# Optimization experiments

Measured on AMD Instinct MI355X. Metric: run time of the kernel, lower is better.

Reference implementation:

```python
import jax, jax.numpy as jnp
import numpy as np

N_SEND = 100000   # sender nodes
N_RECV = 100000   # receiver nodes
E = 600000        # edges
D = 128           # node feature channels (128x0e)
A = 8             # attr channels (8x0e)
S = 64            # edge scalar dim = fc_neurons[0]
H = 128           # fc hidden = fc_neurons[1]; tp.weight_numel = 128
NUM_NEIGHBORS = 32.0
SILU_NORM = 1.679177  # e3nn normalize2mom constant for silu: (E[silu(N(0,1))^2])^-0.5


def fctp(x, y, W):
    """e3nn FullyConnectedTensorProduct for all-scalar (0e) irreps:
    single 'uvw' path, path weight 1/sqrt(mul_u*mul_v)."""
    return jnp.einsum('nu,nv,uvw->nw', x, y, W) / np.sqrt(x.shape[1] * y.shape[1]).astype(np.float32)


def setup_inputs() -> dict:
    key = jax.random.key(0)
    ks = jax.random.split(key, 14)
    return {
        'sender_input': jax.random.normal(ks[0], (N_SEND, D), jnp.float32),
        'sender_attr': jax.random.normal(ks[1], (N_SEND, A), jnp.float32),
        'receiver_input': jax.random.normal(ks[2], (N_RECV, D), jnp.float32),
        'receiver_attr': jax.random.normal(ks[3], (N_RECV, A), jnp.float32),
        'edge_src': jax.random.randint(ks[4], (E,), 0, N_SEND, jnp.int32),
        'edge_dst': jax.random.randint(ks[5], (E,), 0, N_RECV, jnp.int32),
        'edge_attr': jax.random.normal(ks[6], (E, 1), jnp.float32),
        'edge_scalars': jax.random.normal(ks[7], (E, S), jnp.float32),
        # e3nn TP weights are initialized N(0,1)
        'W_sc': jax.random.normal(ks[8], (D, A, D), jnp.float32),
        'W_lin1': jax.random.normal(ks[9], (D, A, D), jnp.float32),
        'W_fc1': jax.random.normal(ks[10], (S, H), jnp.float32),
        'W_fc2': jax.random.normal(ks[11], (H, D), jnp.float32),
        'W_lin2': jax.random.normal(ks[12], (D, A, D), jnp.float32),
        'W_lin3': jax.random.normal(ks[13], (D, A, 1), jnp.float32),
    }


def reference(sender_input, sender_attr, receiver_input, receiver_attr,
              edge_src, edge_dst, edge_attr, edge_scalars,
              W_sc, W_lin1, W_fc1, W_fc2, W_lin2, W_lin3):
    # FullyConnectedNet([S, H, weight_numel], silu): act(x@W/sqrt(fan_in)), last layer linear
    h = SILU_NORM * jax.nn.silu(edge_scalars @ W_fc1 / np.sqrt(S).astype(np.float32))
    weight = h @ W_fc2 / np.sqrt(H).astype(np.float32)                     # [E, D] per-edge TP weights

    receiver_self_connection = fctp(receiver_input, receiver_attr, W_sc)   # [Nr, D]
    sender_features = fctp(sender_input, sender_attr, W_lin1)              # [Ns, D]

    # gather -> per-edge weighted ('uvu') tensor product with 1x0e edge_attr -> scatter-add
    edge_features = weight * sender_features[edge_src] * edge_attr         # [E, D]
    receiver_features = jax.ops.segment_sum(edge_features, edge_dst,
                                            num_segments=receiver_input.shape[0])
    receiver_features = receiver_features / np.sqrt(NUM_NEIGHBORS).astype(np.float32)

    receiver_conv_out = fctp(receiver_features, receiver_attr, W_lin2)     # [Nr, D]
    receiver_angle = 0.1 * fctp(receiver_features, receiver_attr, W_lin3)  # [Nr, 1]
    # sc.output_mask is all-ones for this irreps config, so sin gating applies to all channels
    return jnp.cos(receiver_angle) * receiver_self_connection + jnp.sin(receiver_angle) * receiver_conv_out
```

## Files before the change

### kernel.cpp

```cpp
#include <hip/hip_runtime.h>
#include <hip/hip_bf16.h>
#include <math.h>

#define NS 100000
#define NR 100000
#define NE 600000
#define SILU_NORM 1.679177f

typedef __attribute__((ext_vector_type(8))) short short8;
typedef __attribute__((ext_vector_type(4))) float f32x4;

static __device__ __forceinline__ short f2bf(float f) {
    return __builtin_bit_cast(short, __float2bfloat16(f));
}

#define GLDS16(g, l)                                                         \
    __builtin_amdgcn_global_load_lds(                                        \
        (const __attribute__((address_space(1))) unsigned int*)(const void*)(g), \
        (__attribute__((address_space(3))) unsigned int*)(void*)(l), 16, 0, 0)

__global__ void swz_kernel(const float* __restrict__ W,
                           __hip_bfloat16* __restrict__ out, int total)
{
    int idx = blockIdx.x * 256 + threadIdx.x;
    if (idx >= total) return;
    int s = idx >> 12, r = idx & 4095;
    int f = r >> 9;  r &= 511;
    int quad = r >> 7; r &= 127;
    int wl = r >> 3;
    int j = r & 7;
    int k = s * 32 + quad * 8 + j;
    int w = f * 16 + wl;
    out[idx] = __float2bfloat16(W[(size_t)k * 128 + w]);
}

__global__ __launch_bounds__(256) void hist_kernel(const int* __restrict__ edst,
                                                   int* __restrict__ cnt)
{
    int i = blockIdx.x * 256 + threadIdx.x;
    if (i < NE) atomicAdd(&cnt[edst[i]], 1);
}

#define SCAN_BLK 1024

__global__ __launch_bounds__(256) void scan1_kernel(const int* __restrict__ cnt,
                                                    int* __restrict__ bsum, int n)
{
    __shared__ int ts[256];
    int b = blockIdx.x, t = threadIdx.x;
    int base = b * SCAN_BLK + t * 4;
    int s = 0;
    #pragma unroll
    for (int k = 0; k < 4; ++k) { int i = base + k; if (i < n) s += cnt[i]; }
    ts[t] = s; __syncthreads();
    #pragma unroll
    for (int off = 128; off; off >>= 1) {
        if (t < off) ts[t] += ts[t + off];
        __syncthreads();
    }
    if (t == 0) bsum[b] = ts[0];
}

__global__ __launch_bounds__(128) void scan2_kernel(const int* __restrict__ bsum,
                                                    int* __restrict__ bofs, int nb)
{
    __shared__ int sh[128];
    int t = threadIdx.x;
    sh[t] = (t < nb) ? bsum[t] : 0;
    __syncthreads();
    for (int off = 1; off < 128; off <<= 1) {
        int v = (t >= off) ? sh[t - off] : 0;
        __syncthreads();
        sh[t] += v;
        __syncthreads();
    }
    if (t < nb) bofs[t] = (t == 0) ? 0 : sh[t - 1];
}

__global__ __launch_bounds__(256) void scan3_kernel(const int* __restrict__ cnt,
                                                    const int* __restrict__ bofs,
                                                    int* __restrict__ ofs, int n)
{
    __shared__ int ts[256];
    int b = blockIdx.x, t = threadIdx.x;
    int base = b * SCAN_BLK + t * 4;
    int v[4]; int s = 0;
    #pragma unroll
    for (int k = 0; k < 4; ++k) {
        int i = base + k;
        v[k] = (i < n) ? cnt[i] : 0;
        s += v[k];
    }
    ts[t] = s; __syncthreads();
    for (int off = 1; off < 256; off <<= 1) {
        int u = (t >= off) ? ts[t - off] : 0;
        __syncthreads();
        ts[t] += u;
        __syncthreads();
    }
    int run = bofs[b] + ts[t] - s;
    #pragma unroll
    for (int k = 0; k < 4; ++k) {
        int i = base + k;
        if (i < n) ofs[i] = run;
        run += v[k];
    }
}

__global__ __launch_bounds__(256) void scatter_kernel(const int* __restrict__ edst,
                                                      int* __restrict__ ofs,
                                                      int* __restrict__ perm)
{
    int i = blockIdx.x * 256 + threadIdx.x;
    if (i < NE) {
        int pos = atomicAdd(&ofs[edst[i]], 1);
        perm[pos] = i;
    }
}

__global__ __launch_bounds__(256) void fctp_mfma_kernel(
    const float* __restrict__ x, const float* __restrict__ y,
    const __hip_bfloat16* __restrict__ Wswz, float* __restrict__ out,
    float scale, int N)
{
    __shared__ __hip_bfloat16 Wb[2][8192];
    __shared__ float xs[2][128 * 8];

    const int tid = threadIdx.x;
    const int lane = tid & 63;
    const int wv = tid >> 6;
    const int quad = lane >> 4;
    const int wl = lane & 15;
    const int n0 = blockIdx.x * 128;

    float ya[2][8];
    #pragma unroll
    for (int mt = 0; mt < 2; ++mt) {
        int node = n0 + wv * 32 + mt * 16 + wl;
        if (node >= N) node = N - 1;
        const float4* yp = (const float4*)(y + (size_t)node * 8);
        float4 a = yp[0], b = yp[1];
        ya[mt][0] = a.x; ya[mt][1] = a.y; ya[mt][2] = a.z; ya[mt][3] = a.w;
        ya[mt][4] = b.x; ya[mt][5] = b.y; ya[mt][6] = b.z; ya[mt][7] = b.w;
    }

    f32x4 acc[2][8];
    #pragma unroll
    for (int mt = 0; mt < 2; ++mt)
        #pragma unroll
        for (int f = 0; f < 8; ++f)
            acc[mt][f] = (f32x4){0.f, 0.f, 0.f, 0.f};

    auto stage = [&](int b, int cc) {
        const char* src = (const char*)(Wswz + (size_t)cc * 8192);
        #pragma unroll
        for (int i = 0; i < 4; ++i) {
            int off = (i * 256 + tid) * 16;
            GLDS16(src + off, (char*)Wb[b] + off);
        }
        int nl = tid >> 1, c4 = (tid & 1) * 4;
        int node = n0 + nl;
        if (node >= N) node = N - 1;
        GLDS16(x + (size_t)node * 128 + cc * 8 + c4, (char*)xs[b] + tid * 16);
    };

    stage(0, 0);
    __syncthreads();

    for (int cc = 0; cc < 16; ++cc) {
        int cur = cc & 1;
        if (cc < 15) stage(cur ^ 1, cc + 1);

        #pragma unroll
        for (int ks = 0; ks < 2; ++ks) {
            short8 bfr[8];
            #pragma unroll
            for (int f = 0; f < 8; ++f)
                bfr[f] = *(const short8*)((const short*)Wb[cur] +
                                          (size_t)ks * 4096 + (f * 64 + lane) * 8);
            #pragma unroll
            for (int mt = 0; mt < 2; ++mt) {
                float xv = xs[cur][(wv * 32 + mt * 16 + wl) * 8 + ks * 4 + quad];
                short8 af;
                #pragma unroll
                for (int v = 0; v < 8; ++v) af[v] = f2bf(xv * ya[mt][v]);
                #pragma unroll
                for (int f = 0; f < 8; ++f)
                    acc[mt][f] = __builtin_amdgcn_mfma_f32_16x16x32_bf16(
                        af, bfr[f], acc[mt][f], 0, 0, 0);
            }
        }
        __syncthreads();
    }

    #pragma unroll
    for (int mt = 0; mt < 2; ++mt) {
        #pragma unroll
        for (int r = 0; r < 4; ++r) {
            int node = n0 + wv * 32 + mt * 16 + quad * 4 + r;
            if (node < N) {
                #pragma unroll
                for (int f = 0; f < 8; ++f)
                    out[(size_t)node * 128 + f * 16 + wl] = acc[mt][f][r] * scale;
            }
        }
    }
}

__global__ __launch_bounds__(256, 4) void edge_mfma_kernel(
    const int* __restrict__ esrc, const int* __restrict__ edst,
    const float* __restrict__ eattr, const float* __restrict__ escal,
    const int* __restrict__ perm,
    const __hip_bfloat16* __restrict__ W1swz,
    const __hip_bfloat16* __restrict__ W2swz,
    const float* __restrict__ sf, float* __restrict__ rfeat)
{
    __shared__ __hip_bfloat16 hA[16384];

    const int tid = threadIdx.x;
    const int lane = tid & 63;
    const int wv = tid >> 6;
    const int quad = lane >> 4;
    const int wl = lane & 15;
    const int e0 = blockIdx.x * 128;

    int epm[2];
    #pragma unroll
    for (int mt = 0; mt < 2; ++mt) {
        int j = e0 + (wv * 2 + mt) * 16 + wl;
        if (j >= NE) j = NE - 1;
        epm[mt] = perm[j];
    }

    short8 af1[2][2];
    #pragma unroll
    for (int ks = 0; ks < 2; ++ks)
        #pragma unroll
        for (int mt = 0; mt < 2; ++mt) {
            const float4* p = (const float4*)(escal + (size_t)epm[mt] * 64 +
                                              ks * 32 + quad * 8);
            float4 a = p[0], b = p[1];
            short8 v;
            v[0] = f2bf(a.x); v[1] = f2bf(a.y); v[2] = f2bf(a.z); v[3] = f2bf(a.w);
            v[4] = f2bf(b.x); v[5] = f2bf(b.y); v[6] = f2bf(b.z); v[7] = f2bf(b.w);
            af1[ks][mt] = v;
        }

    f32x4 acc1[2][8];
    #pragma unroll
    for (int mt = 0; mt < 2; ++mt)
        #pragma unroll
        for (int f = 0; f < 8; ++f) acc1[mt][f] = (f32x4){0.f, 0.f, 0.f, 0.f};

    #pragma unroll
    for (int ks = 0; ks < 2; ++ks)
        #pragma unroll
        for (int f = 0; f < 8; ++f) {
            short8 bfr = *(const short8*)((const short*)W1swz +
                                          (size_t)ks * 4096 + (f * 64 + lane) * 8);
            acc1[0][f] = __builtin_amdgcn_mfma_f32_16x16x32_bf16(
                af1[0][0], bfr, acc1[0][f], 0, 0, 0);
            acc1[1][f] = __builtin_amdgcn_mfma_f32_16x16x32_bf16(
                af1[0][1], bfr, acc1[1][f], 0, 0, 0);
        }

    #pragma unroll
    for (int mt = 0; mt < 2; ++mt)
        #pragma unroll
        for (int f = 0; f < 8; ++f) acc1[mt][f] = (f32x4){0.f, 0.f, 0.f, 0.f};
    #pragma unroll
    for (int ks = 0; ks < 2; ++ks)
        #pragma unroll
        for (int f = 0; f < 8; ++f) {
            short8 bfr = *(const short8*)((const short*)W1swz +
                                          (size_t)ks * 4096 + (f * 64 + lane) * 8);
            acc1[0][f] = __builtin_amdgcn_mfma_f32_16x16x32_bf16(
                af1[ks][0], bfr, acc1[0][f], 0, 0, 0);
            acc1[1][f] = __builtin_amdgcn_mfma_f32_16x16x32_bf16(
                af1[ks][1], bfr, acc1[1][f], 0, 0, 0);
        }

    #pragma unroll
    for (int mt = 0; mt < 2; ++mt) {
        int MT = wv * 2 + mt;
        #pragma unroll
        for (int f = 0; f < 8; ++f) {
            int s2 = f >> 1;
            int q2 = ((f & 1) * 2 + (wl >> 3)) & 3;
            int j2 = wl & 7;
            #pragma unroll
            for (int r = 0; r < 4; ++r) {
                float t = acc1[mt][f][r] * 0.125f;
                float h = SILU_NORM * t / (1.f + __expf(-t));
                int lpos = q2 * 16 + quad * 4 + r;
                ((short*)hA)[((size_t)(s2 * 8 + MT) * 64 + lpos) * 8 + j2] = f2bf(h);
            }
        }
    }
    __syncthreads();

    f32x4 acc2[2][8];
    #pragma unroll
    for (int mt = 0; mt < 2; ++mt)
        #pragma unroll
        for (int f = 0; f < 8; ++f) acc2[mt][f] = (f32x4){0.f, 0.f, 0.f, 0.f};

    #pragma unroll
    for (int ks = 0; ks < 4; ++ks) {
        short8 afA = *(const short8*)((const short*)hA +
                                      ((size_t)(ks * 8 + wv * 2 + 0) * 64 + lane) * 8);
        short8 afB = *(const short8*)((const short*)hA +
                                      ((size_t)(ks * 8 + wv * 2 + 1) * 64 + lane) * 8);
        #pragma unroll
        for (int f = 0; f < 8; ++f) {
            short8 bfr = *(const short8*)((const short*)W2swz +
                                          (size_t)ks * 4096 + (f * 64 + lane) * 8);
            acc2[0][f] = __builtin_amdgcn_mfma_f32_16x16x32_bf16(
                afA, bfr, acc2[0][f], 0, 0, 0);
            acc2[1][f] = __builtin_amdgcn_mfma_f32_16x16x32_bf16(
                afB, bfr, acc2[1][f], 0, 0, 0);
        }
    }

    const float s128 = 0.08838834764831845f;
    #pragma unroll
    for (int mt = 0; mt < 2; ++mt) {
        int jbase = e0 + (wv * 2 + mt) * 16 + quad * 4;
        if (jbase < NE) {
            int4 pj = *(const int4*)(perm + jbase);
            int dsts[4], srcs[4];
            float eas[4];
            #pragma unroll
            for (int r = 0; r < 4; ++r) {
                int e = (r == 0) ? pj.x : (r == 1) ? pj.y : (r == 2) ? pj.z : pj.w;
                dsts[r] = edst[e];
                srcs[r] = esrc[e];
                eas[r]  = eattr[e] * s128;
            }
            float run[8];
            int curdst = dsts[0];
            #pragma unroll
            for (int f = 0; f < 8; ++f)
                run[f] = acc2[mt][f][0] * eas[0] *
                         sf[(size_t)srcs[0] * 128 + f * 16 + wl];
            #pragma unroll
            for (int r = 1; r < 4; ++r) {
                float val[8];
                #pragma unroll
                for (int f = 0; f < 8; ++f)
                    val[f] = acc2[mt][f][r] * eas[r] *
                             sf[(size_t)srcs[r] * 128 + f * 16 + wl];
                if (dsts[r] == curdst) {
                    #pragma unroll
                    for (int f = 0; f < 8; ++f) run[f] += val[f];
                } else {
                    #pragma unroll
                    for (int f = 0; f < 8; ++f)
                        atomicAdd(&rfeat[(size_t)curdst * 128 + f * 16 + wl], run[f]);
                    curdst = dsts[r];
                    #pragma unroll
                    for (int f = 0; f < 8; ++f) run[f] = val[f];
                }
            }
            #pragma unroll
            for (int f = 0; f < 8; ++f)
                atomicAdd(&rfeat[(size_t)curdst * 128 + f * 16 + wl], run[f]);
        }
    }
}

__global__ __launch_bounds__(256) void conv_fuse_kernel(
    const float* __restrict__ x, const float* __restrict__ y,
    const __hip_bfloat16* __restrict__ Wswz, const float* __restrict__ W3,
    const float* __restrict__ rsc, float* __restrict__ out, int N)
{
    __shared__ __hip_bfloat16 Wb[2][8192];
    __shared__ float xs[2][128 * 8];

    const int tid = threadIdx.x;
    const int lane = tid & 63;
    const int wv = tid >> 6;
    const int quad = lane >> 4;
    const int wl = lane & 15;
    const int n0 = blockIdx.x * 128;

    float ya[2][8];
    #pragma unroll
    for (int mt = 0; mt < 2; ++mt) {
        int node = n0 + wv * 32 + mt * 16 + wl;
        if (node >= N) node = N - 1;
        const float4* yp = (const float4*)(y + (size_t)node * 8);
        float4 a = yp[0], b = yp[1];
        ya[mt][0] = a.x; ya[mt][1] = a.y; ya[mt][2] = a.z; ya[mt][3] = a.w;
        ya[mt][4] = b.x; ya[mt][5] = b.y; ya[mt][6] = b.z; ya[mt][7] = b.w;
    }

    f32x4 acc[2][8];
    #pragma unroll
    for (int mt = 0; mt < 2; ++mt)
        #pragma unroll
        for (int f = 0; f < 8; ++f)
            acc[mt][f] = (f32x4){0.f, 0.f, 0.f, 0.f};
    float aacc[2] = {0.f, 0.f};

    auto stage = [&](int b, int cc) {
        const char* src = (const char*)(Wswz + (size_t)cc * 8192);
        #pragma unroll
        for (int i = 0; i < 4; ++i) {
            int off = (i * 256 + tid) * 16;
            GLDS16(src + off, (char*)Wb[b] + off);
        }
        int nl = tid >> 1, c4 = (tid & 1) * 4;
        int node = n0 + nl;
        if (node >= N) node = N - 1;
        GLDS16(x + (size_t)node * 128 + cc * 8 + c4, (char*)xs[b] + tid * 16);
    };

    stage(0, 0);
    __syncthreads();

    for (int cc = 0; cc < 16; ++cc) {
        int cur = cc & 1;
        if (cc < 15) stage(cur ^ 1, cc + 1);

        #pragma unroll
        for (int ks = 0; ks < 2; ++ks) {
            short8 bfr[8];
            #pragma unroll
            for (int f = 0; f < 8; ++f)
                bfr[f] = *(const short8*)((const short*)Wb[cur] +
                                          (size_t)ks * 4096 + (f * 64 + lane) * 8);
            const float4* wp = (const float4*)(W3 + ((cc * 8 + ks * 4 + quad) * 8));
            float4 w3a = wp[0], w3b = wp[1];
            float w3v[8] = {w3a.x, w3a.y, w3a.z, w3a.w, w3b.x, w3b.y, w3b.z, w3b.w};
            #pragma unroll
            for (int mt = 0; mt < 2; ++mt) {
                float xv = xs[cur][(wv * 32 + mt * 16 + wl) * 8 + ks * 4 + quad];
                short8 af;
                #pragma unroll
                for (int v = 0; v < 8; ++v) {
                    float pr = xv * ya[mt][v];
                    af[v] = f2bf(pr);
                    aacc[mt] += pr * w3v[v];
                }
                #pragma unroll
                for (int f = 0; f < 8; ++f)
                    acc[mt][f] = __builtin_amdgcn_mfma_f32_16x16x32_bf16(
                        af, bfr[f], acc[mt][f], 0, 0, 0);
            }
        }
        __syncthreads();
    }

    float ared[2];
    #pragma unroll
    for (int mt = 0; mt < 2; ++mt) {
        float a = aacc[mt];
        a += __shfl_xor(a, 16);
        a += __shfl_xor(a, 32);
        ared[mt] = a * 5.524271728019903e-4f;
    }

    const float cs = 5.524271728019903e-3f;
    #pragma unroll
    for (int mt = 0; mt < 2; ++mt) {
        #pragma unroll
        for (int r = 0; r < 4; ++r) {
            int node = n0 + wv * 32 + mt * 16 + quad * 4 + r;
            float a = __shfl(ared[mt], quad * 4 + r);
            if (node < N) {
                float ca = __cosf(a), sa = __sinf(a);
                #pragma unroll
                for (int f = 0; f < 8; ++f) {
                    size_t o = (size_t)node * 128 + f * 16 + wl;
                    out[o] = ca * rsc[o] + sa * (acc[mt][f][r] * cs);
                }
            }
        }
    }
}

extern "C" void kernel_launch(void* const* d_in, const int* in_sizes, int n_in,
                              void* d_out, int out_size, void* d_ws, size_t ws_size,
                              hipStream_t stream)
{
    const float* sender_input   = (const float*)d_in[0];
    const float* sender_attr    = (const float*)d_in[1];
    const float* receiver_input = (const float*)d_in[2];
    const float* receiver_attr  = (const float*)d_in[3];
    const int*   edge_src  = (const int*)d_in[4];
    const int*   edge_dst  = (const int*)d_in[5];
    const float* edge_attr = (const float*)d_in[6];
    const float* edge_scal = (const float*)d_in[7];
    const float* W_sc   = (const float*)d_in[8];
    const float* W_lin1 = (const float*)d_in[9];
    const float* W_fc1  = (const float*)d_in[10];
    const float* W_fc2  = (const float*)d_in[11];
    const float* W_lin2 = (const float*)d_in[12];
    const float* W_lin3 = (const float*)d_in[13];

    char* ws = (char*)d_ws;
    float* sf    = (float*)(ws);
    float* rfeat = (float*)(ws + 51200000);
    __hip_bfloat16* Wl1s = (__hip_bfloat16*)(ws + 102400000);
    __hip_bfloat16* Wscs = (__hip_bfloat16*)(ws + 102662144);
    __hip_bfloat16* Wl2s = (__hip_bfloat16*)(ws + 102924288);
    __hip_bfloat16* W1s  = (__hip_bfloat16*)(ws + 103186432);
    __hip_bfloat16* W2s  = (__hip_bfloat16*)(ws + 103202816);
    float* rsc = sf;

    int* perm = (int*)d_out;
    int* cnt  = (int*)d_out + 600000;
    int* ofs  = (int*)d_out + 700000;
    int* bsum = (int*)d_out + 800000;
    int* bofs = (int*)d_out + 800128;

    swz_kernel<<<512, 256, 0, stream>>>(W_lin1, Wl1s, 131072);
    swz_kernel<<<512, 256, 0, stream>>>(W_sc,   Wscs, 131072);
    swz_kernel<<<512, 256, 0, stream>>>(W_lin2, Wl2s, 131072);
    swz_kernel<<<32,  256, 0, stream>>>(W_fc1,  W1s,  8192);
    swz_kernel<<<64,  256, 0, stream>>>(W_fc2,  W2s,  16384);

    hipMemsetAsync(rfeat, 0, (size_t)NR * 128 * 4, stream);
    hipMemsetAsync(cnt, 0, (size_t)NR * 4, stream);

    const int nbScan = (NR + SCAN_BLK - 1) / SCAN_BLK;
    hist_kernel<<<(NE + 255) / 256, 256, 0, stream>>>(edge_dst, cnt);
    scan1_kernel<<<nbScan, 256, 0, stream>>>(cnt, bsum, NR);
    scan2_kernel<<<1, 128, 0, stream>>>(bsum, bofs, nbScan);
    scan3_kernel<<<nbScan, 256, 0, stream>>>(cnt, bofs, ofs, NR);
    scatter_kernel<<<(NE + 255) / 256, 256, 0, stream>>>(edge_dst, ofs, perm);

    fctp_mfma_kernel<<<(NS + 127) / 128, 256, 0, stream>>>(
        sender_input, sender_attr, Wl1s, sf, 0.03125f, NS);
    edge_mfma_kernel<<<(NE + 127) / 128, 256, 0, stream>>>(
        edge_src, edge_dst, edge_attr, edge_scal, perm, W1s, W2s, sf, rfeat);
    fctp_mfma_kernel<<<(NR + 127) / 128, 256, 0, stream>>>(
        receiver_input, receiver_attr, Wscs, rsc, 0.03125f, NR);
    conv_fuse_kernel<<<(NR + 127) / 128, 256, 0, stream>>>(
        rfeat, receiver_attr, Wl2s, W_lin3, rsc, (float*)d_out, NR);
}
```

Before: 698.3 us.

## Presort edge metadata, vectorize gathers, drop dead MFMA pass, register-based FCTP

The scatter kernel now writes dst, src and edge_attr in sorted order, so the edge kernel loads them contiguously as int4/float4 instead of doing dependent random loads through perm. W_fc2 columns are permuted so each lane owns 8 contiguous output channels, which lets the sender-feature gather use float4 loads. A duplicated first-layer MFMA pass whose result was discarded is removed. The FCTP and conv-fuse kernels drop LDS staging and read weights straight from global memory, with 64 nodes per block. This relies on the cache to serve weight reuse, and the atomics now hit 8 contiguous channels per lane.

```diff
diff --git a/kernel.cpp b/kernel.cpp
--- a/kernel.cpp
+++ b/kernel.cpp
@@ -14,13 +14,9 @@
     return __builtin_bit_cast(short, __float2bfloat16(f));
 }
 
-#define GLDS16(g, l)                                                         \
-    __builtin_amdgcn_global_load_lds(                                        \
-        (const __attribute__((address_space(1))) unsigned int*)(const void*)(g), \
-        (__attribute__((address_space(3))) unsigned int*)(void*)(l), 16, 0, 0)
-
 __global__ void swz_kernel(const float* __restrict__ W,
-                           __hip_bfloat16* __restrict__ out, int total)
+                           __hip_bfloat16* __restrict__ out, int total,
+                           int colperm)
 {
     int idx = blockIdx.x * 256 + threadIdx.x;
     if (idx >= total) return;
@@ -30,7 +26,7 @@
     int wl = r >> 3;
     int j = r & 7;
     int k = s * 32 + quad * 8 + j;
-    int w = f * 16 + wl;
+    int w = colperm ? (wl * 8 + f) : (f * 16 + wl);
     out[idx] = __float2bfloat16(W[(size_t)k * 128 + w]);
 }
 
@@ -107,110 +103,84 @@
     }
 }
 
-__global__ __launch_bounds__(256) void scatter_kernel(const int* __restrict__ edst,
-                                                      int* __restrict__ ofs,
-                                                      int* __restrict__ perm)
+__global__ __launch_bounds__(256) void scatter_kernel(
+    const int* __restrict__ edst, const int* __restrict__ esrc,
+    const float* __restrict__ eattr, int* __restrict__ ofs,
+    int* __restrict__ perm, int* __restrict__ edst_s,
+    int* __restrict__ esrc_s, float* __restrict__ eattr_s)
 {
     int i = blockIdx.x * 256 + threadIdx.x;
     if (i < NE) {
-        int pos = atomicAdd(&ofs[edst[i]], 1);
+        int d = edst[i];
+        int pos = atomicAdd(&ofs[d], 1);
         perm[pos] = i;
-    }
-}
-
-__global__ __launch_bounds__(256) void fctp_mfma_kernel(
+        edst_s[pos] = d;
+        esrc_s[pos] = esrc[i];
+        eattr_s[pos] = eattr[i];
+    }
+}
+
+__global__ __launch_bounds__(256) void fctp_reg_kernel(
     const float* __restrict__ x, const float* __restrict__ y,
     const __hip_bfloat16* __restrict__ Wswz, float* __restrict__ out,
     float scale, int N)
 {
-    __shared__ __hip_bfloat16 Wb[2][8192];
-    __shared__ float xs[2][128 * 8];
-
     const int tid = threadIdx.x;
     const int lane = tid & 63;
     const int wv = tid >> 6;
     const int quad = lane >> 4;
     const int wl = lane & 15;
-    const int n0 = blockIdx.x * 128;
-
-    float ya[2][8];
-    #pragma unroll
-    for (int mt = 0; mt < 2; ++mt) {
-        int node = n0 + wv * 32 + mt * 16 + wl;
-        if (node >= N) node = N - 1;
-        const float4* yp = (const float4*)(y + (size_t)node * 8);
+    const int n0 = blockIdx.x * 64;
+
+    int row = n0 + wv * 16 + wl;
+    if (row >= N) row = N - 1;
+
+    float ya[8];
+    {
+        const float4* yp = (const float4*)(y + (size_t)row * 8);
         float4 a = yp[0], b = yp[1];
-        ya[mt][0] = a.x; ya[mt][1] = a.y; ya[mt][2] = a.z; ya[mt][3] = a.w;
-        ya[mt][4] = b.x; ya[mt][5] = b.y; ya[mt][6] = b.z; ya[mt][7] = b.w;
-    }
-
-    f32x4 acc[2][8];
-    #pragma unroll
-    for (int mt = 0; mt < 2; ++mt)
-        #pragma unroll
-        for (int f = 0; f < 8; ++f)
-            acc[mt][f] = (f32x4){0.f, 0.f, 0.f, 0.f};
-
-    auto stage = [&](int b, int cc) {
-        const char* src = (const char*)(Wswz + (size_t)cc * 8192);
-        #pragma unroll
-        for (int i = 0; i < 4; ++i) {
-            int off = (i * 256 + tid) * 16;
-            GLDS16(src + off, (char*)Wb[b] + off);
-        }
-        int nl = tid >> 1, c4 = (tid & 1) * 4;
-        int node = n0 + nl;
-        if (node >= N) node = N - 1;
-        GLDS16(x + (size_t)node * 128 + cc * 8 + c4, (char*)xs[b] + tid * 16);
-    };
-
-    stage(0, 0);
-    __syncthreads();
-
-    for (int cc = 0; cc < 16; ++cc) {
-        int cur = cc & 1;
-        if (cc < 15) stage(cur ^ 1, cc + 1);
-
-        #pragma unroll
-        for (int ks = 0; ks < 2; ++ks) {
-            short8 bfr[8];
+        ya[0] = a.x; ya[1] = a.y; ya[2] = a.z; ya[3] = a.w;
+        ya[4] = b.x; ya[5] = b.y; ya[6] = b.z; ya[7] = b.w;
+    }
+
+    float xr[32];
+    #pragma unroll
+    for (int j = 0; j < 32; ++j)
+        xr[j] = x[(size_t)row * 128 + quad + 4 * j];
+
+    f32x4 acc[8];
+    #pragma unroll
+    for (int f = 0; f < 8; ++f) acc[f] = (f32x4){0.f, 0.f, 0.f, 0.f};
+
+    #pragma unroll 4
+    for (int s = 0; s < 32; ++s) {
+        float xv = xr[s];
+        short8 af;
+        #pragma unroll
+        for (int v = 0; v < 8; ++v) af[v] = f2bf(xv * ya[v]);
+        #pragma unroll
+        for (int f = 0; f < 8; ++f) {
+            short8 bfr = *(const short8*)((const short*)Wswz +
+                                          (size_t)s * 4096 + (f * 64 + lane) * 8);
+            acc[f] = __builtin_amdgcn_mfma_f32_16x16x32_bf16(af, bfr, acc[f], 0, 0, 0);
+        }
+    }
+
+    #pragma unroll
+    for (int r = 0; r < 4; ++r) {
+        int node = n0 + wv * 16 + quad * 4 + r;
+        if (node < N) {
             #pragma unroll
             for (int f = 0; f < 8; ++f)
-                bfr[f] = *(const short8*)((const short*)Wb[cur] +
-                                          (size_t)ks * 4096 + (f * 64 + lane) * 8);
-            #pragma unroll
-            for (int mt = 0; mt < 2; ++mt) {
-                float xv = xs[cur][(wv * 32 + mt * 16 + wl) * 8 + ks * 4 + quad];
-                short8 af;
-                #pragma unroll
-                for (int v = 0; v < 8; ++v) af[v] = f2bf(xv * ya[mt][v]);
-                #pragma unroll
-                for (int f = 0; f < 8; ++f)
-                    acc[mt][f] = __builtin_amdgcn_mfma_f32_16x16x32_bf16(
-                        af, bfr[f], acc[mt][f], 0, 0, 0);
-            }
-        }
-        __syncthreads();
-    }
-
-    #pragma unroll
-    for (int mt = 0; mt < 2; ++mt) {
-        #pragma unroll
-        for (int r = 0; r < 4; ++r) {
-            int node = n0 + wv * 32 + mt * 16 + quad * 4 + r;
-            if (node < N) {
-                #pragma unroll
-                for (int f = 0; f < 8; ++f)
-                    out[(size_t)node * 128 + f * 16 + wl] = acc[mt][f][r] * scale;
-            }
+                out[(size_t)node * 128 + f * 16 + wl] = acc[f][r] * scale;
         }
     }
 }
 
 __global__ __launch_bounds__(256, 4) void edge_mfma_kernel(
-    const int* __restrict__ esrc, const int* __restrict__ edst,
-    const float* __restrict__ eattr, const float* __restrict__ escal,
-    const int* __restrict__ perm,
+    const int* __restrict__ perm, const int* __restrict__ edst_s,
+    const int* __restrict__ esrc_s, const float* __restrict__ eattr_s,
+    const float* __restrict__ escal,
     const __hip_bfloat16* __restrict__ W1swz,
     const __hip_bfloat16* __restrict__ W2swz,
     const float* __restrict__ sf, float* __restrict__ rfeat)
@@ -230,6 +200,20 @@
         int j = e0 + (wv * 2 + mt) * 16 + wl;
         if (j >= NE) j = NE - 1;
         epm[mt] = perm[j];
+    }
+
+    const float s128 = 0.08838834764831845f;
+    int4 dstv[2], srcv[2];
+    float4 eav[2];
+    bool valid[2];
+    #pragma unroll
+    for (int mt = 0; mt < 2; ++mt) {
+        int jb = e0 + (wv * 2 + mt) * 16 + quad * 4;
+        valid[mt] = (jb < NE);
+        int jc = valid[mt] ? jb : 0;
+        dstv[mt] = *(const int4*)(edst_s + jc);
+        srcv[mt] = *(const int4*)(esrc_s + jc);
+        eav[mt]  = *(const float4*)(eattr_s + jc);
     }
 
     short8 af1[2][2];
@@ -252,22 +236,6 @@
         #pragma unroll
         for (int f = 0; f < 8; ++f) acc1[mt][f] = (f32x4){0.f, 0.f, 0.f, 0.f};
 
-    #pragma unroll
-    for (int ks = 0; ks < 2; ++ks)
-        #pragma unroll
-        for (int f = 0; f < 8; ++f) {
-            short8 bfr = *(const short8*)((const short*)W1swz +
-                                          (size_t)ks * 4096 + (f * 64 + lane) * 8);
-            acc1[0][f] = __builtin_amdgcn_mfma_f32_16x16x32_bf16(
-                af1[0][0], bfr, acc1[0][f], 0, 0, 0);
-            acc1[1][f] = __builtin_amdgcn_mfma_f32_16x16x32_bf16(
-                af1[0][1], bfr, acc1[1][f], 0, 0, 0);
-        }
-
-    #pragma unroll
-    for (int mt = 0; mt < 2; ++mt)
-        #pragma unroll
-        for (int f = 0; f < 8; ++f) acc1[mt][f] = (f32x4){0.f, 0.f, 0.f, 0.f};
     #pragma unroll
     for (int ks = 0; ks < 2; ++ks)
         #pragma unroll
@@ -322,50 +290,50 @@
         }
     }
 
-    const float s128 = 0.08838834764831845f;
     #pragma unroll
     for (int mt = 0; mt < 2; ++mt) {
-        int jbase = e0 + (wv * 2 + mt) * 16 + quad * 4;
-        if (jbase < NE) {
-            int4 pj = *(const int4*)(perm + jbase);
-            int dsts[4], srcs[4];
-            float eas[4];
+        if (!valid[mt]) continue;
+        int dsts[4] = {dstv[mt].x, dstv[mt].y, dstv[mt].z, dstv[mt].w};
+        int srcs[4] = {srcv[mt].x, srcv[mt].y, srcv[mt].z, srcv[mt].w};
+        float eas[4] = {eav[mt].x * s128, eav[mt].y * s128,
+                        eav[mt].z * s128, eav[mt].w * s128};
+        float4 g0[4], g1[4];
+        #pragma unroll
+        for (int r = 0; r < 4; ++r) {
+            const float4* gp = (const float4*)(sf + (size_t)srcs[r] * 128 + wl * 8);
+            g0[r] = gp[0];
+            g1[r] = gp[1];
+        }
+        float run[8];
+        int curdst = dsts[0];
+        #pragma unroll
+        for (int j = 0; j < 8; ++j) {
+            float g = (j < 4) ? ((const float*)&g0[0])[j] : ((const float*)&g1[0])[j - 4];
+            run[j] = acc2[mt][j][0] * eas[0] * g;
+        }
+        #pragma unroll
+        for (int r = 1; r < 4; ++r) {
+            float val[8];
             #pragma unroll
-            for (int r = 0; r < 4; ++r) {
-                int e = (r == 0) ? pj.x : (r == 1) ? pj.y : (r == 2) ? pj.z : pj.w;
-                dsts[r] = edst[e];
-                srcs[r] = esrc[e];
-                eas[r]  = eattr[e] * s128;
+            for (int j = 0; j < 8; ++j) {
+                float g = (j < 4) ? ((const float*)&g0[r])[j] : ((const float*)&g1[r])[j - 4];
+                val[j] = acc2[mt][j][r] * eas[r] * g;
             }
-            float run[8];
-            int curdst = dsts[0];
-            #pragma unroll
-            for (int f = 0; f < 8; ++f)
-                run[f] = acc2[mt][f][0] * eas[0] *
-                         sf[(size_t)srcs[0] * 128 + f * 16 + wl];
-            #pragma unroll
-            for (int r = 1; r < 4; ++r) {
-                float val[8];
+            if (dsts[r] == curdst) {
                 #pragma unroll
-                for (int f = 0; f < 8; ++f)
-                    val[f] = acc2[mt][f][r] * eas[r] *
-                             sf[(size_t)srcs[r] * 128 + f * 16 + wl];
-                if (dsts[r] == curdst) {
-                    #pragma unroll
-                    for (int f = 0; f < 8; ++f) run[f] += val[f];
-                } else {
-                    #pragma unroll
-                    for (int f = 0; f < 8; ++f)
-                        atomicAdd(&rfeat[(size_t)curdst * 128 + f * 16 + wl], run[f]);
-                    curdst = dsts[r];
-                    #pragma unroll
-                    for (int f = 0; f < 8; ++f) run[f] = val[f];
-                }
+                for (int j = 0; j < 8; ++j) run[j] += val[j];
+            } else {
+                #pragma unroll
+                for (int j = 0; j < 8; ++j)
+                    atomicAdd(&rfeat[(size_t)curdst * 128 + wl * 8 + j], run[j]);
+                curdst = dsts[r];
+                #pragma unroll
+                for (int j = 0; j < 8; ++j) run[j] = val[j];
             }
-            #pragma unroll
-            for (int f = 0; f < 8; ++f)
-                atomicAdd(&rfeat[(size_t)curdst * 128 + f * 16 + wl], run[f]);
-        }
+        }
+        #pragma unroll
+        for (int j = 0; j < 8; ++j)
+            atomicAdd(&rfeat[(size_t)curdst * 128 + wl * 8 + j], run[j]);
     }
 }
 
@@ -374,107 +342,71 @@
     const __hip_bfloat16* __restrict__ Wswz, const float* __restrict__ W3,
     const float* __restrict__ rsc, float* __restrict__ out, int N)
 {
-    __shared__ __hip_bfloat16 Wb[2][8192];
-    __shared__ float xs[2][128 * 8];
-
     const int tid = threadIdx.x;
     const int lane = tid & 63;
     const int wv = tid >> 6;
     const int quad = lane >> 4;
     const int wl = lane & 15;
-    const int n0 = blockIdx.x * 128;
-
-    float ya[2][8];
-    #pragma unroll
-    for (int mt = 0; mt < 2; ++mt) {
-        int node = n0 + wv * 32 + mt * 16 + wl;
-        if (node >= N) node = N - 1;
-        const float4* yp = (const float4*)(y + (size_t)node * 8);
+    const int n0 = blockIdx.x * 64;
+
+    int row = n0 + wv * 16 + wl;
+    if (row >= N) row = N - 1;
+
+    float ya[8];
+    {
+        const float4* yp = (const float4*)(y + (size_t)row * 8);
         float4 a = yp[0], b = yp[1];
-        ya[mt][0] = a.x; ya[mt][1] = a.y; ya[mt][2] = a.z; ya[mt][3] = a.w;
-        ya[mt][4] = b.x; ya[mt][5] = b.y; ya[mt][6] = b.z; ya[mt][7] = b.w;
-    }
-
-    f32x4 acc[2][8];
-    #pragma unroll
-    for (int mt = 0; mt < 2; ++mt)
-        #pragma unroll
-        for (int f = 0; f < 8; ++f)
-            acc[mt][f] = (f32x4){0.f, 0.f, 0.f, 0.f};
-    float aacc[2] = {0.f, 0.f};
-
-    auto stage = [&](int b, int cc) {
-        const char* src = (const char*)(Wswz + (size_t)cc * 8192);
-        #pragma unroll
-        for (int i = 0; i < 4; ++i) {
-            int off = (i * 256 + tid) * 16;
-            GLDS16(src + off, (char*)Wb[b] + off);
-        }
-        int nl = tid >> 1, c4 = (tid & 1) * 4;
-        int node = n0 + nl;
-        if (node >= N) node = N - 1;
-        GLDS16(x + (size_t)node * 128 + cc * 8 + c4, (char*)xs[b] + tid * 16);
-    };
-
-    stage(0, 0);
-    __syncthreads();
-
-    for (int cc = 0; cc < 16; ++cc) {
-        int cur = cc & 1;
-        if (cc < 15) stage(cur ^ 1, cc + 1);
-
-        #pragma unroll
-        for (int ks = 0; ks < 2; ++ks) {
-            short8 bfr[8];
+        ya[0] = a.x; ya[1] = a.y; ya[2] = a.z; ya[3] = a.w;
+        ya[4] = b.x; ya[5] = b.y; ya[6] = b.z; ya[7] = b.w;
+    }
+
+    float xr[32];
+    #pragma unroll
+    for (int j = 0; j < 32; ++j)
+        xr[j] = x[(size_t)row * 128 + quad + 4 * j];
+
+    f32x4 acc[8];
+    #pragma unroll
+    for (int f = 0; f < 8; ++f) acc[f] = (f32x4){0.f, 0.f, 0.f, 0.f};
+    float aacc = 0.f;
+
+    #pragma unroll 4
+    for (int s = 0; s < 32; ++s) {
+        float xv = xr[s];
+        const float4* wp = (const float4*)(W3 + (s * 4 + quad) * 8);
+        float4 w3a = wp[0], w3b = wp[1];
+        float w3v[8] = {w3a.x, w3a.y, w3a.z, w3a.w, w3b.x, w3b.y, w3b.z, w3b.w};
+        short8 af;
+        #pragma unroll
+        for (int v = 0; v < 8; ++v) {
+            float pr = xv * ya[v];
+            af[v] = f2bf(pr);
+            aacc += pr * w3v[v];
+        }
+        #pragma unroll
+        for (int f = 0; f < 8; ++f) {
+            short8 bfr = *(const short8*)((const short*)Wswz +
+                                          (size_t)s * 4096 + (f * 64 + lane) * 8);
+            acc[f] = __builtin_amdgcn_mfma_f32_16x16x32_bf16(af, bfr, acc[f], 0, 0, 0);
+        }
+    }
+
+    float a = aacc;
+    a += __shfl_xor(a, 16);
+    a += __shfl_xor(a, 32);
+    float ared = a * 5.524271728019903e-4f;
+
+    const float cs = 5.524271728019903e-3f;
+    #pragma unroll
+    for (int r = 0; r < 4; ++r) {
+        int node = n0 + wv * 16 + quad * 4 + r;
+        float an = __shfl(ared, quad * 4 + r);
+        if (node < N) {
+            float ca = __cosf(an), sa = __sinf(an);
             #pragma unroll
-            for (int f = 0; f < 8; ++f)
-                bfr[f] = *(const short8*)((const short*)Wb[cur] +
-                                          (size_t)ks * 4096 + (f * 64 + lane) * 8);
-            const float4* wp = (const float4*)(W3 + ((cc * 8 + ks * 4 + quad) * 8));
-            float4 w3a = wp[0], w3b = wp[1];
-            float w3v[8] = {w3a.x, w3a.y, w3a.z, w3a.w, w3b.x, w3b.y, w3b.z, w3b.w};
-            #pragma unroll
-            for (int mt = 0; mt < 2; ++mt) {
-                float xv = xs[cur][(wv * 32 + mt * 16 + wl) * 8 + ks * 4 + quad];
-                short8 af;
-                #pragma unroll
-                for (int v = 0; v < 8; ++v) {
-                    float pr = xv * ya[mt][v];
-                    af[v] = f2bf(pr);
-                    aacc[mt] += pr * w3v[v];
-                }
-                #pragma unroll
-                for (int f = 0; f < 8; ++f)
-                    acc[mt][f] = __builtin_amdgcn_mfma_f32_16x16x32_bf16(
-                        af, bfr[f], acc[mt][f], 0, 0, 0);
-            }
-        }
-        __syncthreads();
-    }
-
-    float ared[2];
-    #pragma unroll
-    for (int mt = 0; mt < 2; ++mt) {
-        float a = aacc[mt];
-        a += __shfl_xor(a, 16);
-        a += __shfl_xor(a, 32);
-        ared[mt] = a * 5.524271728019903e-4f;
-    }
-
-    const float cs = 5.524271728019903e-3f;
-    #pragma unroll
-    for (int mt = 0; mt < 2; ++mt) {
-        #pragma unroll
-        for (int r = 0; r < 4; ++r) {
-            int node = n0 + wv * 32 + mt * 16 + quad * 4 + r;
-            float a = __shfl(ared[mt], quad * 4 + r);
-            if (node < N) {
-                float ca = __cosf(a), sa = __sinf(a);
-                #pragma unroll
-                for (int f = 0; f < 8; ++f) {
-                    size_t o = (size_t)node * 128 + f * 16 + wl;
-                    out[o] = ca * rsc[o] + sa * (acc[mt][f][r] * cs);
-                }
+            for (int f = 0; f < 8; ++f) {
+                size_t o = (size_t)node * 128 + f * 16 + wl;
+                out[o] = ca * rsc[o] + sa * (acc[f][r] * cs);
             }
         }
     }
@@ -509,17 +441,20 @@
     __hip_bfloat16* W2s  = (__hip_bfloat16*)(ws + 103202816);
     float* rsc = sf;
 
-    int* perm = (int*)d_out;
-    int* cnt  = (int*)d_out + 600000;
-    int* ofs  = (int*)d_out + 700000;
-    int* bsum = (int*)d_out + 800000;
-    int* bofs = (int*)d_out + 800128;
-
-    swz_kernel<<<512, 256, 0, stream>>>(W_lin1, Wl1s, 131072);
-    swz_kernel<<<512, 256, 0, stream>>>(W_sc,   Wscs, 131072);
-    swz_kernel<<<512, 256, 0, stream>>>(W_lin2, Wl2s, 131072);
-    swz_kernel<<<32,  256, 0, stream>>>(W_fc1,  W1s,  8192);
-    swz_kernel<<<64,  256, 0, stream>>>(W_fc2,  W2s,  16384);
+    int*   perm    = (int*)d_out;
+    int*   edst_s  = (int*)d_out + 600000;
+    int*   esrc_s  = (int*)d_out + 1200000;
+    float* eattr_s = (float*)d_out + 1800000;
+    int*   cnt     = (int*)d_out + 2400000;
+    int*   ofs     = (int*)d_out + 2500000;
+    int*   bsum    = (int*)d_out + 2600000;
+    int*   bofs    = (int*)d_out + 2600128;
+
+    swz_kernel<<<512, 256, 0, stream>>>(W_lin1, Wl1s, 131072, 0);
+    swz_kernel<<<512, 256, 0, stream>>>(W_sc,   Wscs, 131072, 0);
+    swz_kernel<<<512, 256, 0, stream>>>(W_lin2, Wl2s, 131072, 0);
+    swz_kernel<<<32,  256, 0, stream>>>(W_fc1,  W1s,  8192,  0);
+    swz_kernel<<<64,  256, 0, stream>>>(W_fc2,  W2s,  16384, 1);
 
     hipMemsetAsync(rfeat, 0, (size_t)NR * 128 * 4, stream);
     hipMemsetAsync(cnt, 0, (size_t)NR * 4, stream);
@@ -529,14 +464,15 @@
     scan1_kernel<<<nbScan, 256, 0, stream>>>(cnt, bsum, NR);
     scan2_kernel<<<1, 128, 0, stream>>>(bsum, bofs, nbScan);
     scan3_kernel<<<nbScan, 256, 0, stream>>>(cnt, bofs, ofs, NR);
-    scatter_kernel<<<(NE + 255) / 256, 256, 0, stream>>>(edge_dst, ofs, perm);
-
-    fctp_mfma_kernel<<<(NS + 127) / 128, 256, 0, stream>>>(
+    scatter_kernel<<<(NE + 255) / 256, 256, 0, stream>>>(
+        edge_dst, edge_src, edge_attr, ofs, perm, edst_s, esrc_s, eattr_s);
+
+    fctp_reg_kernel<<<(NS + 63) / 64, 256, 0, stream>>>(
         sender_input, sender_attr, Wl1s, sf, 0.03125f, NS);
     edge_mfma_kernel<<<(NE + 127) / 128, 256, 0, stream>>>(
-        edge_src, edge_dst, edge_attr, edge_scal, perm, W1s, W2s, sf, rfeat);
-    fctp_mfma_kernel<<<(NR + 127) / 128, 256, 0, stream>>>(
+        perm, edst_s, esrc_s, eattr_s, edge_scal, W1s, W2s, sf, rfeat);
+    fctp_reg_kernel<<<(NR + 63) / 64, 256, 0, stream>>>(
         receiver_input, receiver_attr, Wscs, rsc, 0.03125f, NR);
-    conv_fuse_kernel<<<(NR + 127) / 128, 256, 0, stream>>>(
+    conv_fuse_kernel<<<(NR + 63) / 64, 256, 0, stream>>>(
         rfeat, receiver_attr, Wl2s, W_lin3, rsc, (float*)d_out, NR);
 }
```

After: 1.763 ms. 2.52x slower.

## Presort edge metadata, drop duplicate fc1 pass, fuse receiver self-connection into conv

Applied to the files above, without the earlier changes.

The scatter kernel now also writes dst, src and edge_attr into destination-sorted arrays, so the edge kernel reads them with contiguous int4/float4 loads instead of going through perm indirection. It also hoists these loads and all source-feature gathers ahead of the atomic segment reduction. A redundant first fc1 MFMA pass, whose result was immediately zeroed, is removed. The receiver self-connection fctp is merged into the final conv kernel, which computes both products in one pass and avoids writing and rereading the rsc intermediate, at the cost of doubled LDS use and more registers that may lower occupancy.

```diff
diff --git a/kernel.cpp b/kernel.cpp
--- a/kernel.cpp
+++ b/kernel.cpp
@@ -107,14 +107,20 @@
     }
 }
 
-__global__ __launch_bounds__(256) void scatter_kernel(const int* __restrict__ edst,
-                                                      int* __restrict__ ofs,
-                                                      int* __restrict__ perm)
+__global__ __launch_bounds__(256) void scatter_kernel(
+    const int* __restrict__ edst, const int* __restrict__ esrc,
+    const float* __restrict__ eattr, int* __restrict__ ofs,
+    int* __restrict__ perm, int* __restrict__ edst_s,
+    int* __restrict__ esrc_s, float* __restrict__ eattr_s)
 {
     int i = blockIdx.x * 256 + threadIdx.x;
     if (i < NE) {
-        int pos = atomicAdd(&ofs[edst[i]], 1);
+        int d = edst[i];
+        int pos = atomicAdd(&ofs[d], 1);
         perm[pos] = i;
+        edst_s[pos] = d;
+        esrc_s[pos] = esrc[i];
+        eattr_s[pos] = eattr[i];
     }
 }
 
@@ -201,16 +207,16 @@
             if (node < N) {
                 #pragma unroll
                 for (int f = 0; f < 8; ++f)
-                    out[(size_t)node * 128 + f * 16 + wl] = acc[mt][f][r] * scale;
+                    out[(size_t)node * 128 + f * 16 + wl] = acc[f != f ? 0 : mt][f][r] * scale;
             }
         }
     }
 }
 
 __global__ __launch_bounds__(256, 4) void edge_mfma_kernel(
-    const int* __restrict__ esrc, const int* __restrict__ edst,
-    const float* __restrict__ eattr, const float* __restrict__ escal,
-    const int* __restrict__ perm,
+    const int* __restrict__ perm, const int* __restrict__ edst_s,
+    const int* __restrict__ esrc_s, const float* __restrict__ eattr_s,
+    const float* __restrict__ escal,
     const __hip_bfloat16* __restrict__ W1swz,
     const __hip_bfloat16* __restrict__ W2swz,
     const float* __restrict__ sf, float* __restrict__ rfeat)
@@ -230,6 +236,20 @@
         int j = e0 + (wv * 2 + mt) * 16 + wl;
         if (j >= NE) j = NE - 1;
         epm[mt] = perm[j];
+    }
+
+    const float s128 = 0.08838834764831845f;
+    int4 dstv[2], srcv[2];
+    float4 eav[2];
+    bool valid[2];
+    #pragma unroll
+    for (int mt = 0; mt < 2; ++mt) {
+        int jb = e0 + (wv * 2 + mt) * 16 + quad * 4;
+        valid[mt] = (jb < NE);
+        int jc = valid[mt] ? jb : 0;
+        dstv[mt] = *(const int4*)(edst_s + jc);
+        srcv[mt] = *(const int4*)(esrc_s + jc);
+        eav[mt]  = *(const float4*)(eattr_s + jc);
     }
 
     short8 af1[2][2];
@@ -252,22 +272,6 @@
         #pragma unroll
         for (int f = 0; f < 8; ++f) acc1[mt][f] = (f32x4){0.f, 0.f, 0.f, 0.f};
 
-    #pragma unroll
-    for (int ks = 0; ks < 2; ++ks)
-        #pragma unroll
-        for (int f = 0; f < 8; ++f) {
-            short8 bfr = *(const short8*)((const short*)W1swz +
-                                          (size_t)ks * 4096 + (f * 64 + lane) * 8);
-            acc1[0][f] = __builtin_amdgcn_mfma_f32_16x16x32_bf16(
-                af1[0][0], bfr, acc1[0][f], 0, 0, 0);
-            acc1[1][f] = __builtin_amdgcn_mfma_f32_16x16x32_bf16(
-                af1[0][1], bfr, acc1[1][f], 0, 0, 0);
-        }
-
-    #pragma unroll
-    for (int mt = 0; mt < 2; ++mt)
-        #pragma unroll
-        for (int f = 0; f < 8; ++f) acc1[mt][f] = (f32x4){0.f, 0.f, 0.f, 0.f};
     #pragma unroll
     for (int ks = 0; ks < 2; ++ks)
         #pragma unroll
@@ -322,60 +326,62 @@
         }
     }
 
-    const float s128 = 0.08838834764831845f;
-    #pragma unroll
-    for (int mt = 0; mt < 2; ++mt) {
-        int jbase = e0 + (wv * 2 + mt) * 16 + quad * 4;
-        if (jbase < NE) {
-            int4 pj = *(const int4*)(perm + jbase);
-            int dsts[4], srcs[4];
-            float eas[4];
-            #pragma unroll
-            for (int r = 0; r < 4; ++r) {
-                int e = (r == 0) ? pj.x : (r == 1) ? pj.y : (r == 2) ? pj.z : pj.w;
-                dsts[r] = edst[e];
-                srcs[r] = esrc[e];
-                eas[r]  = eattr[e] * s128;
-            }
-            float run[8];
-            int curdst = dsts[0];
+    #pragma unroll
+    for (int mt = 0; mt < 2; ++mt) {
+        if (!valid[mt]) continue;
+        int dsts[4] = {dstv[mt].x, dstv[mt].y, dstv[mt].z, dstv[mt].w};
+        int srcs[4] = {srcv[mt].x, srcv[mt].y, srcv[mt].z, srcv[mt].w};
+        float eas[4] = {eav[mt].x * s128, eav[mt].y * s128,
+                        eav[mt].z * s128, eav[mt].w * s128};
+        float g[4][8];
+        #pragma unroll
+        for (int r = 0; r < 4; ++r)
             #pragma unroll
             for (int f = 0; f < 8; ++f)
-                run[f] = acc2[mt][f][0] * eas[0] *
-                         sf[(size_t)srcs[0] * 128 + f * 16 + wl];
-            #pragma unroll
-            for (int r = 1; r < 4; ++r) {
-                float val[8];
-                #pragma unroll
-                for (int f = 0; f < 8; ++f)
-                    val[f] = acc2[mt][f][r] * eas[r] *
-                             sf[(size_t)srcs[r] * 128 + f * 16 + wl];
-                if (dsts[r] == curdst) {
-                    #pragma unroll
-                    for (int f = 0; f < 8; ++f) run[f] += val[f];
-                } else {
-                    #pragma unroll
-                    for (int f = 0; f < 8; ++f)
-                        atomicAdd(&rfeat[(size_t)curdst * 128 + f * 16 + wl], run[f]);
-                    curdst = dsts[r];
-                    #pragma unroll
-                    for (int f = 0; f < 8; ++f) run[f] = val[f];
-                }
-            }
+                g[r][f] = sf[(size_t)srcs[r] * 128 + f * 16 + wl];
+
+        float run[8];
+        int curdst = dsts[0];
+        #pragma unroll
+        for (int f = 0; f < 8; ++f)
+            run[f] = acc2[mt][f][0] * eas[0] * g[0][f];
+        #pragma unroll
+        for (int r = 1; r < 4; ++r) {
+            float val[8];
             #pragma unroll
             for (int f = 0; f < 8; ++f)
-                atomicAdd(&rfeat[(size_t)curdst * 128 + f * 16 + wl], run[f]);
-        }
-    }
-}
-
-__global__ __launch_bounds__(256) void conv_fuse_kernel(
-    const float* __restrict__ x, const float* __restrict__ y,
-    const __hip_bfloat16* __restrict__ Wswz, const float* __restrict__ W3,
-    const float* __restrict__ rsc, float* __restrict__ out, int N)
-{
-    __shared__ __hip_bfloat16 Wb[2][8192];
-    __shared__ float xs[2][128 * 8];
+                val[f] = acc2[mt][f][r] * eas[r] * g[r][f];
+            if (dsts[r] == curdst) {
+                #pragma unroll
+                for (int f = 0; f < 8; ++f) run[f] += val[f];
+            } else {
+                #pragma unroll
+                for (int f = 0; f < 8; ++f)
+                    atomicAdd(&rfeat[(size_t)curdst * 128 + f * 16 + wl], run[f]);
+                curdst = dsts[r];
+                #pragma unroll
+                for (int f = 0; f < 8; ++f) run[f] = val[f];
+            }
+        }
+        #pragma unroll
+        for (int f = 0; f < 8; ++f)
+            atomicAdd(&rfeat[(size_t)curdst * 128 + f * 16 + wl], run[f]);
+    }
+}
+
+__global__ __launch_bounds__(256) void recv_fuse_kernel(
+    const float* __restrict__ xin,
+    const float* __restrict__ xrf,
+    const float* __restrict__ y,
+    const __hip_bfloat16* __restrict__ WscS,
+    const __hip_bfloat16* __restrict__ Wl2S,
+    const float* __restrict__ W3,
+    float* __restrict__ out, int N)
+{
+    __shared__ __hip_bfloat16 WbA[2][8192];
+    __shared__ __hip_bfloat16 WbB[2][8192];
+    __shared__ float xsA[2][128 * 8];
+    __shared__ float xsB[2][128 * 8];
 
     const int tid = threadIdx.x;
     const int lane = tid & 63;
@@ -395,25 +401,30 @@
         ya[mt][4] = b.x; ya[mt][5] = b.y; ya[mt][6] = b.z; ya[mt][7] = b.w;
     }
 
-    f32x4 acc[2][8];
+    f32x4 accA[2][8], accB[2][8];
     #pragma unroll
     for (int mt = 0; mt < 2; ++mt)
         #pragma unroll
-        for (int f = 0; f < 8; ++f)
-            acc[mt][f] = (f32x4){0.f, 0.f, 0.f, 0.f};
+        for (int f = 0; f < 8; ++f) {
+            accA[mt][f] = (f32x4){0.f, 0.f, 0.f, 0.f};
+            accB[mt][f] = (f32x4){0.f, 0.f, 0.f, 0.f};
+        }
     float aacc[2] = {0.f, 0.f};
 
     auto stage = [&](int b, int cc) {
-        const char* src = (const char*)(Wswz + (size_t)cc * 8192);
+        const char* sA = (const char*)(WscS + (size_t)cc * 8192);
+        const char* sB = (const char*)(Wl2S + (size_t)cc * 8192);
         #pragma unroll
         for (int i = 0; i < 4; ++i) {
             int off = (i * 256 + tid) * 16;
-            GLDS16(src + off, (char*)Wb[b] + off);
+            GLDS16(sA + off, (char*)WbA[b] + off);
+            GLDS16(sB + off, (char*)WbB[b] + off);
         }
         int nl = tid >> 1, c4 = (tid & 1) * 4;
         int node = n0 + nl;
         if (node >= N) node = N - 1;
-        GLDS16(x + (size_t)node * 128 + cc * 8 + c4, (char*)xs[b] + tid * 16);
+        GLDS16(xin + (size_t)node * 128 + cc * 8 + c4, (char*)xsA[b] + tid * 16);
+        GLDS16(xrf + (size_t)node * 128 + cc * 8 + c4, (char*)xsB[b] + tid * 16);
     };
 
     stage(0, 0);
@@ -425,28 +436,49 @@
 
         #pragma unroll
         for (int ks = 0; ks < 2; ++ks) {
-            short8 bfr[8];
-            #pragma unroll
-            for (int f = 0; f < 8; ++f)
-                bfr[f] = *(const short8*)((const short*)Wb[cur] +
-                                          (size_t)ks * 4096 + (f * 64 + lane) * 8);
-            const float4* wp = (const float4*)(W3 + ((cc * 8 + ks * 4 + quad) * 8));
-            float4 w3a = wp[0], w3b = wp[1];
-            float w3v[8] = {w3a.x, w3a.y, w3a.z, w3a.w, w3b.x, w3b.y, w3b.z, w3b.w};
-            #pragma unroll
-            for (int mt = 0; mt < 2; ++mt) {
-                float xv = xs[cur][(wv * 32 + mt * 16 + wl) * 8 + ks * 4 + quad];
-                short8 af;
-                #pragma unroll
-                for (int v = 0; v < 8; ++v) {
-                    float pr = xv * ya[mt][v];
-                    af[v] = f2bf(pr);
-                    aacc[mt] += pr * w3v[v];
+            {
+                short8 bfr[8];
+                #pragma unroll
+                for (int f = 0; f < 8; ++f)
+                    bfr[f] = *(const short8*)((const short*)WbA[cur] +
+                                              (size_t)ks * 4096 + (f * 64 + lane) * 8);
+                #pragma unroll
+                for (int mt = 0; mt < 2; ++mt) {
+                    float xv = xsA[cur][(wv * 32 + mt * 16 + wl) * 8 + ks * 4 + quad];
+                    short8 af;
+                    #pragma unroll
+                    for (int v = 0; v < 8; ++v) af[v] = f2bf(xv * ya[mt][v]);
+                    #pragma unroll
+                    for (int f = 0; f < 8; ++f)
+                        accA[mt][f] = __builtin_amdgcn_mfma_f32_16x16x32_bf16(
+                            af, bfr[f], accA[mt][f], 0, 0, 0);
                 }
+            }
+            {
+                short8 bfr[8];
                 #pragma unroll
                 for (int f = 0; f < 8; ++f)
-                    acc[mt][f] = __builtin_amdgcn_mfma_f32_16x16x32_bf16(
-                        af, bfr[f], acc[mt][f], 0, 0, 0);
+                    bfr[f] = *(const short8*)((const short*)WbB[cur] +
+                                              (size_t)ks * 4096 + (f * 64 + lane) * 8);
+                const float4* wp = (const float4*)(W3 + ((cc * 8 + ks * 4 + quad) * 8));
+                float4 w3a = wp[0], w3b = wp[1];
+                float w3v[8] = {w3a.x, w3a.y, w3a.z, w3a.w,
+                                w3b.x, w3b.y, w3b.z, w3b.w};
+                #pragma unroll
+                for (int mt = 0; mt < 2; ++mt) {
+                    float xv = xsB[cur][(wv * 32 + mt * 16 + wl) * 8 + ks * 4 + quad];
+                    short8 af;
+                    #pragma unroll
+                    for (int v = 0; v < 8; ++v) {
+                        float pr = xv * ya[mt][v];
+                        af[v] = f2bf(pr);
+                        aacc[mt] += pr * w3v[v];
+                    }
+                    #pragma unroll
+                    for (int f = 0; f < 8; ++f)
+                        accB[mt][f] = __builtin_amdgcn_mfma_f32_16x16x32_bf16(
+                            af, bfr[f], accB[mt][f], 0, 0, 0);
+                }
             }
         }
         __syncthreads();
@@ -461,19 +493,21 @@
         ared[mt] = a * 5.524271728019903e-4f;
     }
 
-    const float cs = 5.524271728019903e-3f;
+    const float csB = 5.524271728019903e-3f;
+    const float csA = 0.03125f;
     #pragma unroll
     for (int mt = 0; mt < 2; ++mt) {
         #pragma unroll
         for (int r = 0; r < 4; ++r) {
             int node = n0 + wv * 32 + mt * 16 + quad * 4 + r;
-            float a = __shfl(ared[mt], quad * 4 + r);
+            float an = __shfl(ared[mt], quad * 4 + r);
             if (node < N) {
-                float ca = __cosf(a), sa = __sinf(a);
+                float ca = __cosf(an), sa = __sinf(an);
                 #pragma unroll
                 for (int f = 0; f < 8; ++f) {
                     size_t o = (size_t)node * 128 + f * 16 + wl;
-                    out[o] = ca * rsc[o] + sa * (acc[mt][f][r] * cs);
+                    out[o] = ca * (accA[mt][f][r] * csA) +
+                             sa * (accB[mt][f][r] * csB);
                 }
             }
         }
@@ -507,13 +541,15 @@
     __hip_bfloat16* Wl2s = (__hip_bfloat16*)(ws + 102924288);
     __hip_bfloat16* W1s  = (__hip_bfloat16*)(ws + 103186432);
     __hip_bfloat16* W2s  = (__hip_bfloat16*)(ws + 103202816);
-    float* rsc = sf;
-
-    int* perm = (int*)d_out;
-    int* cnt  = (int*)d_out + 600000;
-    int* ofs  = (int*)d_out + 700000;
-    int* bsum = (int*)d_out + 800000;
-    int* bofs = (int*)d_out + 800128;
+
+    int*   perm    = (int*)d_out;
+    int*   edst_s  = (int*)d_out + 600000;
+    int*   esrc_s  = (int*)d_out + 1200000;
+    float* eattr_s = (float*)d_out + 1800000;
+    int*   cnt     = (int*)d_out + 2400000;
+    int*   ofs     = (int*)d_out + 2500000;
+    int*   bsum    = (int*)d_out + 2600000;
+    int*   bofs    = (int*)d_out + 2600128;
 
     swz_kernel<<<512, 256, 0, stream>>>(W_lin1, Wl1s, 131072);
     swz_kernel<<<512, 256, 0, stream>>>(W_sc,   Wscs, 131072);
@@ -529,14 +565,14 @@
     scan1_kernel<<<nbScan, 256, 0, stream>>>(cnt, bsum, NR);
     scan2_kernel<<<1, 128, 0, stream>>>(bsum, bofs, nbScan);
     scan3_kernel<<<nbScan, 256, 0, stream>>>(cnt, bofs, ofs, NR);
-    scatter_kernel<<<(NE + 255) / 256, 256, 0, stream>>>(edge_dst, ofs, perm);
+    scatter_kernel<<<(NE + 255) / 256, 256, 0, stream>>>(
+        edge_dst, edge_src, edge_attr, ofs, perm, edst_s, esrc_s, eattr_s);
 
     fctp_mfma_kernel<<<(NS + 127) / 128, 256, 0, stream>>>(
         sender_input, sender_attr, Wl1s, sf, 0.03125f, NS);
     edge_mfma_kernel<<<(NE + 127) / 128, 256, 0, stream>>>(
-        edge_src, edge_dst, edge_attr, edge_scal, perm, W1s, W2s, sf, rfeat);
-    fctp_mfma_kernel<<<(NR + 127) / 128, 256, 0, stream>>>(
-        receiver_input, receiver_attr, Wscs, rsc, 0.03125f, NR);
-    conv_fuse_kernel<<<(NR + 127) / 128, 256, 0, stream>>>(
-        rfeat, receiver_attr, Wl2s, W_lin3, rsc, (float*)d_out, NR);
-}
+        perm, edst_s, esrc_s, eattr_s, edge_scal, W1s, W2s, sf, rfeat);
+    recv_fuse_kernel<<<(NR + 127) / 128, 256, 0, stream>>>(
+        receiver_input, rfeat, receiver_attr, Wscs, Wl2s, W_lin3,
+        (float*)d_out, NR);
+}
```

New measurement: 773.8 us. +10.8%, slower.
